# Kernel tuning notes

Hardware: AMD Instinct MI355X
Metric: run time of the kernel (lower is better)

The kernel has to match this reference:

```python
import jax, jax.numpy as jnp
import numpy as np

NOOBJ_LAMBDA = 0.5
COORD_LAMBDA = 5.0


def _cxcywh_to_xyxy(b):
    cx, cy, w, h = b[..., 0], b[..., 1], b[..., 2], b[..., 3]
    return jnp.stack([cx - w / 2, cy - h / 2, cx + w / 2, cy + h / 2], axis=-1)


def _pairwise_iou(a, b):
    # a: [B, N, 4] xyxy (preds), b: [B, M, 4] xyxy (targets) -> [B, N, M]
    lt = jnp.maximum(a[:, :, None, :2], b[:, None, :, :2])
    rb = jnp.minimum(a[:, :, None, 2:], b[:, None, :, 2:])
    wh = jnp.clip(rb - lt, 0.0)
    inter = wh[..., 0] * wh[..., 1]
    area_a = (a[..., 2] - a[..., 0]) * (a[..., 3] - a[..., 1])
    area_b = (b[..., 2] - b[..., 0]) * (b[..., 3] - b[..., 1])
    union = area_a[:, :, None] + area_b[:, None, :] - inter
    return inter / jnp.where(union > 0, union, 1.0)


def setup_inputs() -> dict:
    key = jax.random.key(0)
    kp, kt, km = jax.random.split(key, 3)
    B = 8192
    # positive values so sqrt(w), sqrt(h) is well-defined (as the torch code assumes)
    pred = jax.random.uniform(kp, (B, 7, 7, 30), dtype=jnp.float32, minval=0.05, maxval=1.0)
    target = jax.random.uniform(kt, (B, 7, 7, 30), dtype=jnp.float32, minval=0.05, maxval=1.0)
    # target confidence channel (index 4) is the obj/noobj indicator: 0 or 1
    obj = (jax.random.uniform(km, (B, 7, 7)) < 0.2).astype(jnp.float32)
    target = target.at[..., 4].set(obj)
    return {"pred_tensor": pred, "target_tensor": target}


def reference(pred_tensor, target_tensor):
    B = pred_tensor.shape[0]
    pred = pred_tensor.reshape(B, 49, 30)
    target = target_tensor.reshape(B, 49, 30)

    conf_t = target[..., 4]            # [B,49]
    noobj = conf_t == 0                # [B,49]
    obj = conf_t > 0                   # [B,49]

    # --- no-object confidence loss (channels 4 and 9) ---
    d4 = pred[..., 4] - target[..., 4]
    d9 = pred[..., 9] - target[..., 9]
    noobj_loss = jnp.sum(jnp.where(noobj, d4 * d4 + d9 * d9, 0.0))

    # --- object cells: 2 boxes per cell, padded to all 49 cells with a mask ---
    pb = pred[..., :10].reshape(B, 98, 5)
    tb = target[..., :10].reshape(B, 98, 5)
    box_mask = jnp.repeat(obj, 2, axis=1)  # [B,98]

    p_xyxy = _cxcywh_to_xyxy(pb[..., :4])
    t_xyxy = _cxcywh_to_xyxy(tb[..., :4])
    iou = _pairwise_iou(p_xyxy, t_xyxy)  # [B,98,98]
    pair_mask = box_mask[:, :, None] & box_mask[:, None, :]
    iou = jnp.where(pair_mask, iou, 0.0)
    max_iou = jnp.max(iou, axis=1)       # max over pred boxes, per target box [B,98]
    cmask = (max_iou != 0) & box_mask    # [B,98]

    cm = cmask.astype(pred.dtype)
    # coord (cx,cy) loss
    dxy = pb[..., :2] - tb[..., :2]
    coord_loss_cxcy = jnp.sum(cm * jnp.sum(dxy * dxy, axis=-1))
    # coord (sqrt w, sqrt h) loss
    dwh = jnp.sqrt(pb[..., 2:4]) - jnp.sqrt(tb[..., 2:4])
    coord_loss_wh = jnp.sum(cm * jnp.sum(dwh * dwh, axis=-1))
    # object confidence loss
    dconf = pb[..., 4] - tb[..., 4]
    obj_loss = jnp.sum(cm * dconf * dconf)

    # --- class loss over object cells ---
    dcls = pred[..., 10:] - target[..., 10:]
    cls_loss = jnp.sum(obj.astype(pred.dtype) * jnp.sum(dcls * dcls, axis=-1))

    bsz = jnp.asarray(B, pred.dtype)
    batch_cls_loss = cls_loss / bsz
    batch_obj_loss = (obj_loss + noobj_loss * NOOBJ_LAMBDA) / bsz
    batch_coord_loss = (coord_loss_cxcy + coord_loss_wh) * COORD_LAMBDA / bsz
    batch_loss = batch_cls_loss + batch_obj_loss + batch_coord_loss
    return (batch_loss, batch_cls_loss, batch_obj_loss, batch_coord_loss)
```

## Files before the change

### kernel.cpp

```cpp
#include <hip/hip_runtime.h>

#define CELLS 49
#define CH 30
#define ROW (CELLS * CH)

__device__ __forceinline__ float waveReduce(float v) {
    #pragma unroll
    for (int o = 32; o > 0; o >>= 1) v += __shfl_xor(v, o, 64);
    return v;
}

__global__ __launch_bounds__(64) void yolo_main(const float* __restrict__ pred,
                                                const float* __restrict__ targ,
                                                float* __restrict__ ws, int B) {
    const int b = blockIdx.x;
    const int tid = threadIdx.x;

    __shared__ float sp[ROW];
    __shared__ float st[ROW];
    __shared__ int cellList[CELLS];
    __shared__ float bx1[2 * CELLS], by1[2 * CELLS], bx2[2 * CELLS], by2[2 * CELLS];

    const float2* p2 = (const float2*)(pred + (size_t)b * ROW);
    const float2* t2 = (const float2*)(targ + (size_t)b * ROW);
    float2* sp2 = (float2*)sp;
    float2* st2 = (float2*)st;
    #pragma unroll
    for (int i = tid; i < ROW / 2; i += 64) {
        sp2[i] = p2[i];
        st2[i] = t2[i];
    }
    __syncthreads();

    float cls = 0.f, objc = 0.f, coord = 0.f;

    bool isObj = false;
    if (tid < CELLS) {
        const int base = tid * CH;
        const float ct = st[base + 4];
        isObj = ct > 0.f;
        if (!isObj) {
            float d4 = sp[base + 4] - ct;
            float d9 = sp[base + 9] - st[base + 9];
            objc += 0.5f * (d4 * d4 + d9 * d9);
        } else {
            #pragma unroll
            for (int k = 10; k < CH; ++k) {
                float d = sp[base + k] - st[base + k];
                cls += d * d;
            }
        }
    }

    unsigned long long m = __ballot(isObj);
    int nObj = __popcll(m);
    if (isObj) {
        int pos = __popcll(m & ((1ull << tid) - 1ull));
        cellList[pos] = tid;
    }
    __syncthreads();

    const int nBox = 2 * nObj;

    for (int e = tid; e < nBox; e += 64) {
        const int c = cellList[e >> 1];
        const int base = c * CH + (e & 1) * 5;
        float cx = sp[base], cy = sp[base + 1], w = sp[base + 2], h = sp[base + 3];
        bx1[e] = cx - 0.5f * w;
        by1[e] = cy - 0.5f * h;
        bx2[e] = cx + 0.5f * w;
        by2[e] = cy + 0.5f * h;
    }
    __syncthreads();

    for (int e = tid; e < nBox; e += 64) {
        const int c = cellList[e >> 1];
        const int base = c * CH + (e & 1) * 5;
        const float tcx = st[base], tcy = st[base + 1];
        const float tw = st[base + 2], th = st[base + 3];
        const float tx1 = tcx - 0.5f * tw, ty1 = tcy - 0.5f * th;
        const float tx2 = tcx + 0.5f * tw, ty2 = tcy + 0.5f * th;
        const float ta = (tx2 - tx1) * (ty2 - ty1);

        float maxiou = 0.f;
        for (int i = 0; i < nBox; ++i) {
            float lx = fmaxf(bx1[i], tx1), ly = fmaxf(by1[i], ty1);
            float rx = fminf(bx2[i], tx2), ry = fminf(by2[i], ty2);
            float iw = fmaxf(rx - lx, 0.f), ih = fmaxf(ry - ly, 0.f);
            float inter = iw * ih;
            float pa = (bx2[i] - bx1[i]) * (by2[i] - by1[i]);
            float un = pa + ta - inter;
            float iou = inter / (un > 0.f ? un : 1.f);
            maxiou = fmaxf(maxiou, iou);
        }

        if (maxiou != 0.f) {
            float dcx = sp[base] - tcx;
            float dcy = sp[base + 1] - tcy;
            coord += dcx * dcx + dcy * dcy;
            float dw = sqrtf(sp[base + 2]) - sqrtf(tw);
            float dh = sqrtf(sp[base + 3]) - sqrtf(th);
            coord += dw * dw + dh * dh;
            float dc = sp[base + 4] - st[base + 4];
            objc += dc * dc;
        }
    }

    cls = waveReduce(cls);
    objc = waveReduce(objc);
    coord = waveReduce(coord);
    if (tid == 0) {
        ws[b] = cls;
        ws[B + b] = objc;
        ws[2 * B + b] = coord;
    }
}

__global__ __launch_bounds__(256) void yolo_reduce(const float* __restrict__ ws,
                                                   float* __restrict__ out, int B) {
    const int tid = threadIdx.x;
    float cls = 0.f, objc = 0.f, coord = 0.f;
    for (int i = tid; i < B; i += 256) {
        cls += ws[i];
        objc += ws[B + i];
        coord += ws[2 * B + i];
    }
    __shared__ float red[3][4];
    cls = waveReduce(cls);
    objc = waveReduce(objc);
    coord = waveReduce(coord);
    const int wave = tid >> 6;
    if ((tid & 63) == 0) {
        red[0][wave] = cls;
        red[1][wave] = objc;
        red[2][wave] = coord;
    }
    __syncthreads();
    if (tid == 0) {
        float c = red[0][0] + red[0][1] + red[0][2] + red[0][3];
        float o = red[1][0] + red[1][1] + red[1][2] + red[1][3];
        float x = red[2][0] + red[2][1] + red[2][2] + red[2][3];
        const float invB = 1.0f / (float)B;
        float bcls = c * invB;
        float bobj = o * invB;
        float bcoord = x * 5.0f * invB;
        out[0] = bcls + bobj + bcoord;
        out[1] = bcls;
        out[2] = bobj;
        out[3] = bcoord;
    }
}

extern "C" void kernel_launch(void* const* d_in, const int* in_sizes, int n_in,
                              void* d_out, int out_size, void* d_ws, size_t ws_size,
                              hipStream_t stream) {
    const float* pred = (const float*)d_in[0];
    const float* targ = (const float*)d_in[1];
    float* ws = (float*)d_ws;
    float* out = (float*)d_out;
    const int B = in_sizes[0] / ROW;

    yolo_main<<<B, 64, 0, stream>>>(pred, targ, ws, B);
    yolo_reduce<<<1, 256, 0, stream>>>(ws, out, B);
}
```

Baseline: 142.9 us.

## Read cells directly from global and pack four rows per block

Drops the staging of whole pred/target rows into shared memory. Each lane now loads only the channels it needs straight from global memory, and four batch rows run as separate waves in one 256-thread block, with predicted boxes kept as float4 in shared memory. Per-block partials are combined in shared memory before the write, and the final reduction uses a 1024-thread block over fewer partials. The cost is strided, partly uncoalesced global loads that rely on the cache to pick up the remaining channels of each cell.

```diff
diff --git a/kernel.cpp b/kernel.cpp
--- a/kernel.cpp
+++ b/kernel.cpp
@@ -1,8 +1,9 @@
 #include <hip/hip_runtime.h>
 
+#define CH 30
 #define CELLS 49
-#define CH 30
 #define ROW (CELLS * CH)
+#define RPB 4
 
 __device__ __forceinline__ float waveReduce(float v) {
     #pragma unroll
@@ -10,140 +11,135 @@
     return v;
 }
 
-__global__ __launch_bounds__(64) void yolo_main(const float* __restrict__ pred,
-                                                const float* __restrict__ targ,
-                                                float* __restrict__ ws, int B) {
-    const int b = blockIdx.x;
-    const int tid = threadIdx.x;
+__global__ __launch_bounds__(256) void yolo_main(const float* __restrict__ pred,
+                                                 const float* __restrict__ targ,
+                                                 float* __restrict__ ws,
+                                                 int B, int NB) {
+    const int w = threadIdx.x >> 6;
+    const int lane = threadIdx.x & 63;
+    const int r = blockIdx.x * RPB + w;
 
-    __shared__ float sp[ROW];
-    __shared__ float st[ROW];
-    __shared__ int cellList[CELLS];
-    __shared__ float bx1[2 * CELLS], by1[2 * CELLS], bx2[2 * CELLS], by2[2 * CELLS];
+    __shared__ float4 boxS[RPB][98];
+    __shared__ int clist[RPB][49];
+    __shared__ float partial[RPB][3];
 
-    const float2* p2 = (const float2*)(pred + (size_t)b * ROW);
-    const float2* t2 = (const float2*)(targ + (size_t)b * ROW);
-    float2* sp2 = (float2*)sp;
-    float2* st2 = (float2*)st;
-    #pragma unroll
-    for (int i = tid; i < ROW / 2; i += 64) {
-        sp2[i] = p2[i];
-        st2[i] = t2[i];
-    }
-    __syncthreads();
+    const float* P = pred + (size_t)r * ROW;
+    const float* T = targ + (size_t)r * ROW;
+    const bool act = (lane < CELLS) && (r < B);
 
     float cls = 0.f, objc = 0.f, coord = 0.f;
+    bool isObj = false;
 
-    bool isObj = false;
-    if (tid < CELLS) {
-        const int base = tid * CH;
-        const float ct = st[base + 4];
-        isObj = ct > 0.f;
+    if (act) {
+        const int cb = lane * CH;
+        const float t4 = T[cb + 4];
+        const float p4 = P[cb + 4];
+        const float p9 = P[cb + 9];
+        const float t9 = T[cb + 9];
+        isObj = t4 > 0.f;
         if (!isObj) {
-            float d4 = sp[base + 4] - ct;
-            float d9 = sp[base + 9] - st[base + 9];
-            objc += 0.5f * (d4 * d4 + d9 * d9);
+            const float d9 = p9 - t9;
+            objc = 0.5f * (p4 * p4 + d9 * d9);
         } else {
+            const float2* pc = (const float2*)(P + cb + 10);
+            const float2* tc = (const float2*)(T + cb + 10);
             #pragma unroll
-            for (int k = 10; k < CH; ++k) {
-                float d = sp[base + k] - st[base + k];
-                cls += d * d;
+            for (int k = 0; k < 10; ++k) {
+                const float2 a = pc[k], b2 = tc[k];
+                const float dx = a.x - b2.x, dy = a.y - b2.y;
+                cls += dx * dx + dy * dy;
             }
         }
     }
 
-    unsigned long long m = __ballot(isObj);
-    int nObj = __popcll(m);
+    const unsigned long long m = __ballot(isObj);
+    const int nObj = __popcll(m);
     if (isObj) {
-        int pos = __popcll(m & ((1ull << tid) - 1ull));
-        cellList[pos] = tid;
+        const int pos = __popcll(m & ((1ull << lane) - 1ull));
+        clist[w][pos] = lane;
     }
     __syncthreads();
 
     const int nBox = 2 * nObj;
 
-    for (int e = tid; e < nBox; e += 64) {
-        const int c = cellList[e >> 1];
-        const int base = c * CH + (e & 1) * 5;
-        float cx = sp[base], cy = sp[base + 1], w = sp[base + 2], h = sp[base + 3];
-        bx1[e] = cx - 0.5f * w;
-        by1[e] = cy - 0.5f * h;
-        bx2[e] = cx + 0.5f * w;
-        by2[e] = cy + 0.5f * h;
+    for (int e = lane; e < nBox; e += 64) {
+        const int c = clist[w][e >> 1];
+        const float* pb = P + c * CH + (e & 1) * 5;
+        const float cx = pb[0], cy = pb[1], bw = pb[2], bh = pb[3];
+        boxS[w][e] = make_float4(cx - 0.5f * bw, cy - 0.5f * bh,
+                                 cx + 0.5f * bw, cy + 0.5f * bh);
     }
     __syncthreads();
 
-    for (int e = tid; e < nBox; e += 64) {
-        const int c = cellList[e >> 1];
-        const int base = c * CH + (e & 1) * 5;
-        const float tcx = st[base], tcy = st[base + 1];
-        const float tw = st[base + 2], th = st[base + 3];
+    for (int e = lane; e < nBox; e += 64) {
+        const int c = clist[w][e >> 1];
+        const int bb = c * CH + (e & 1) * 5;
+        const float tcx = T[bb], tcy = T[bb + 1], tw = T[bb + 2], th = T[bb + 3];
         const float tx1 = tcx - 0.5f * tw, ty1 = tcy - 0.5f * th;
         const float tx2 = tcx + 0.5f * tw, ty2 = tcy + 0.5f * th;
         const float ta = (tx2 - tx1) * (ty2 - ty1);
-
         float maxiou = 0.f;
         for (int i = 0; i < nBox; ++i) {
-            float lx = fmaxf(bx1[i], tx1), ly = fmaxf(by1[i], ty1);
-            float rx = fminf(bx2[i], tx2), ry = fminf(by2[i], ty2);
-            float iw = fmaxf(rx - lx, 0.f), ih = fmaxf(ry - ly, 0.f);
-            float inter = iw * ih;
-            float pa = (bx2[i] - bx1[i]) * (by2[i] - by1[i]);
-            float un = pa + ta - inter;
-            float iou = inter / (un > 0.f ? un : 1.f);
+            const float4 pb4 = boxS[w][i];
+            const float lx = fmaxf(pb4.x, tx1), ly = fmaxf(pb4.y, ty1);
+            const float rx = fminf(pb4.z, tx2), ry = fminf(pb4.w, ty2);
+            const float iw = fmaxf(rx - lx, 0.f), ih = fmaxf(ry - ly, 0.f);
+            const float inter = iw * ih;
+            const float pa = (pb4.z - pb4.x) * (pb4.w - pb4.y);
+            const float un = pa + ta - inter;
+            const float iou = inter / (un > 0.f ? un : 1.f);
             maxiou = fmaxf(maxiou, iou);
         }
-
         if (maxiou != 0.f) {
-            float dcx = sp[base] - tcx;
-            float dcy = sp[base + 1] - tcy;
+            const float dcx = P[bb] - tcx, dcy = P[bb + 1] - tcy;
             coord += dcx * dcx + dcy * dcy;
-            float dw = sqrtf(sp[base + 2]) - sqrtf(tw);
-            float dh = sqrtf(sp[base + 3]) - sqrtf(th);
+            const float dw = sqrtf(P[bb + 2]) - sqrtf(tw);
+            const float dh = sqrtf(P[bb + 3]) - sqrtf(th);
             coord += dw * dw + dh * dh;
-            float dc = sp[base + 4] - st[base + 4];
+            const float dc = P[bb + 4] - T[bb + 4];
             objc += dc * dc;
         }
     }
 
-    cls = waveReduce(cls);
-    objc = waveReduce(objc);
-    coord = waveReduce(coord);
-    if (tid == 0) {
-        ws[b] = cls;
-        ws[B + b] = objc;
-        ws[2 * B + b] = coord;
+    cls = waveReduce(cls); objc = waveReduce(objc); coord = waveReduce(coord);
+    if (lane == 0) { partial[w][0] = cls; partial[w][1] = objc; partial[w][2] = coord; }
+    __syncthreads();
+    if (threadIdx.x == 0) {
+        float c = 0.f, o = 0.f, x = 0.f;
+        #pragma unroll
+        for (int i = 0; i < RPB; ++i) { c += partial[i][0]; o += partial[i][1]; x += partial[i][2]; }
+        ws[blockIdx.x] = c;
+        ws[NB + blockIdx.x] = o;
+        ws[2 * NB + blockIdx.x] = x;
     }
 }
 
-__global__ __launch_bounds__(256) void yolo_reduce(const float* __restrict__ ws,
-                                                   float* __restrict__ out, int B) {
+__global__ __launch_bounds__(1024) void yolo_reduce(const float* __restrict__ ws,
+                                                    float* __restrict__ out,
+                                                    int NB, float invB) {
     const int tid = threadIdx.x;
-    float cls = 0.f, objc = 0.f, coord = 0.f;
-    for (int i = tid; i < B; i += 256) {
-        cls += ws[i];
-        objc += ws[B + i];
-        coord += ws[2 * B + i];
+    const int w = tid >> 6, lane = tid & 63;
+    __shared__ float sred[16];
+    __shared__ float sums[3];
+    #pragma unroll
+    for (int s = 0; s < 3; ++s) {
+        float v = 0.f;
+        for (int i = tid; i < NB; i += 1024) v += ws[s * NB + i];
+        v = waveReduce(v);
+        if (lane == 0) sred[w] = v;
+        __syncthreads();
+        if (tid == 0) {
+            float t = 0.f;
+            #pragma unroll
+            for (int k = 0; k < 16; ++k) t += sred[k];
+            sums[s] = t;
+        }
+        __syncthreads();
     }
-    __shared__ float red[3][4];
-    cls = waveReduce(cls);
-    objc = waveReduce(objc);
-    coord = waveReduce(coord);
-    const int wave = tid >> 6;
-    if ((tid & 63) == 0) {
-        red[0][wave] = cls;
-        red[1][wave] = objc;
-        red[2][wave] = coord;
-    }
-    __syncthreads();
     if (tid == 0) {
-        float c = red[0][0] + red[0][1] + red[0][2] + red[0][3];
-        float o = red[1][0] + red[1][1] + red[1][2] + red[1][3];
-        float x = red[2][0] + red[2][1] + red[2][2] + red[2][3];
-        const float invB = 1.0f / (float)B;
-        float bcls = c * invB;
-        float bobj = o * invB;
-        float bcoord = x * 5.0f * invB;
+        const float bcls = sums[0] * invB;
+        const float bobj = sums[1] * invB;
+        const float bcoord = sums[2] * 5.0f * invB;
         out[0] = bcls + bobj + bcoord;
         out[1] = bcls;
         out[2] = bobj;
@@ -159,7 +155,8 @@
     float* ws = (float*)d_ws;
     float* out = (float*)d_out;
     const int B = in_sizes[0] / ROW;
+    const int NB = (B + RPB - 1) / RPB;
 
-    yolo_main<<<B, 64, 0, stream>>>(pred, targ, ws, B);
-    yolo_reduce<<<1, 256, 0, stream>>>(ws, out, B);
+    yolo_main<<<NB, 256, 0, stream>>>(pred, targ, ws, B, NB);
+    yolo_reduce<<<1, 1024, 0, stream>>>(ws, out, NB, 1.0f / (float)B);
 }
```

Measured after the change: 126.0 us. 1.13x faster.
